# Kernel optimization log

Hardware: AMD Instinct MI355X
Metric: run time of the kernel (lower is better)

Reference implementation:

```python
import jax, jax.numpy as jnp
import numpy as np

D_MODEL = 1024
NUM_HEADS = 16
HEAD_DIM = D_MODEL // NUM_HEADS


def setup_inputs() -> dict:
    key = jax.random.key(0)
    ks = jax.random.split(key, 6)
    B, S = 2, 2048
    s = 1.0 / np.sqrt(D_MODEL)
    return {
        "x": jax.random.normal(ks[0], (B, S, D_MODEL), dtype=jnp.float32),
        "Wq": jax.random.normal(ks[1], (D_MODEL, D_MODEL), dtype=jnp.float32) * s,
        "Wk": jax.random.normal(ks[2], (D_MODEL, D_MODEL), dtype=jnp.float32) * s,
        "Wv": jax.random.normal(ks[3], (D_MODEL, D_MODEL), dtype=jnp.float32) * s,
        "Wo": jax.random.normal(ks[4], (D_MODEL, D_MODEL), dtype=jnp.float32) * s,
        "bo": jax.random.normal(ks[5], (D_MODEL,), dtype=jnp.float32) * 0.01,
    }


def reference(x, Wq, Wk, Wv, Wo, bo):
    b, n, _ = x.shape
    # QKV projections (no bias, qkv_bias=False); weights applied as x @ W^T like nn.Linear
    q = (x @ Wq.T).reshape(b, n, NUM_HEADS, HEAD_DIM).transpose(0, 2, 1, 3)  # [b,h,n,d]
    k = (x @ Wk.T).reshape(b, n, NUM_HEADS, HEAD_DIM).transpose(0, 2, 1, 3)
    v = (x @ Wv.T).reshape(b, n, NUM_HEADS, HEAD_DIM).transpose(0, 2, 1, 3)
    scores = jnp.einsum("bhqd,bhkd->bhqk", q, k)
    causal = jnp.tril(jnp.ones((n, n), dtype=bool))  # keep where True
    scores = jnp.where(causal, scores, -jnp.inf)
    weights = jax.nn.softmax(scores / np.sqrt(HEAD_DIM), axis=-1)
    # dropout p=0.0 -> identity (eval semantics)
    ctx = jnp.einsum("bhqk,bhkd->bhqd", weights, v)
    ctx = ctx.transpose(0, 2, 1, 3).reshape(b, n, D_MODEL)
    return ctx @ Wo.T + bo
```

## Files before the change

kernel.cpp:

```cpp
#include <hip/hip_runtime.h>

#define D_MODEL 1024
#define NUM_HEADS 16
#define HEAD_DIM 64
#define BATCH 2
#define SEQ 2048
#define MTOT (BATCH * SEQ)

typedef __attribute__((ext_vector_type(8))) short bf16x8;
typedef __attribute__((ext_vector_type(4))) short s16x4;
typedef __attribute__((ext_vector_type(4))) float f32x4;
typedef unsigned short u16;
typedef unsigned long long u64;

__device__ __forceinline__ u16 f2bf(float f) {
    unsigned u = __float_as_uint(f);
    return (u16)((u + 0x7FFFu + ((u >> 16) & 1u)) >> 16);
}
__device__ __forceinline__ float bf2f(u16 v) {
    return __uint_as_float((unsigned)v << 16);
}

__device__ __forceinline__ unsigned cvt_pk_bf16(float lo, float hi) {
    unsigned r;
    asm volatile("v_cvt_pk_bf16_f32 %0, %1, %2" : "=v"(r) : "v"(lo), "v"(hi));
    return r;
}

#if __has_builtin(__builtin_amdgcn_exp2f)
#define EXP2(x) __builtin_amdgcn_exp2f(x)
#else
#define EXP2(x) exp2f(x)
#endif

#define GLOAD16(gp, lp) __builtin_amdgcn_global_load_lds(                      \
    (const __attribute__((address_space(1))) void*)(gp),                       \
    (__attribute__((address_space(3))) void*)(lp), 16, 0, 0)

__global__ __launch_bounds__(256)
void cast_all_kernel(const float* __restrict__ x,  const float* __restrict__ Wq,
                     const float* __restrict__ Wk, const float* __restrict__ Wv,
                     const float* __restrict__ Wo, u16* __restrict__ dst)
{
    const int i = blockIdx.x * 256 + threadIdx.x;
    const float* src;
    int j;
    if (i < 524288) { src = x; j = i; }
    else if (i < 917504) {
        const int k = i - 524288;
        const int z = k >> 17;
        src = (z == 0) ? Wq : (z == 1) ? Wk : Wv;
        j = k & 0x1FFFF;
    } else { src = Wo; j = i - 917504; }
    const float4* s = reinterpret_cast<const float4*>(src) + (size_t)j * 2;
    float4 a = s[0], b = s[1];
    u16 tmp[8] = {f2bf(a.x), f2bf(a.y), f2bf(a.z), f2bf(a.w),
                  f2bf(b.x), f2bf(b.y), f2bf(b.z), f2bf(b.w)};
    *reinterpret_cast<int4*>(dst + (size_t)i * 8) = *reinterpret_cast<int4*>(tmp);
}

__global__ __launch_bounds__(256)
void gemm_qkv_kernel(const u16* __restrict__ A, const u16* __restrict__ B,
                     u16* __restrict__ Qo, u16* __restrict__ Ko, u16* __restrict__ Vt)
{
    __shared__ u16 Al[128 * 64];
    __shared__ u16 Bl[128 * 64];

    const int tid = threadIdx.x;
    const int l = tid & 63;
    const int w = tid >> 6;
    const int wm = w >> 1, wn = w & 1;
    const int lr = l & 15, lg = l >> 4;
    const int m0 = blockIdx.y * 128;
    const int n0 = blockIdx.x * 128;

    const int srow = tid >> 3;
    const int scol = ((tid & 7) ^ (srow & 7)) * 8;
    const int sxa = (lr & 7) * 8;

    f32x4 acc[4][4];
    #pragma unroll
    for (int i = 0; i < 4; ++i)
        #pragma unroll
        for (int j = 0; j < 4; ++j) acc[i][j] = (f32x4){0.f, 0.f, 0.f, 0.f};

    for (int k0 = 0; k0 < D_MODEL; k0 += 64) {
        __syncthreads();
        #pragma unroll
        for (int i = 0; i < 4; ++i) {
            const u16* ga = A + (size_t)(m0 + i * 32 + srow) * D_MODEL + k0 + scol;
            const u16* gb = B + (size_t)(n0 + i * 32 + srow) * D_MODEL + k0 + scol;
            GLOAD16(ga, Al + i * 2048 + w * 512);
            GLOAD16(gb, Bl + i * 2048 + w * 512);
        }
        __syncthreads();
        #pragma unroll
        for (int kc = 0; kc < 2; ++kc) {
            bf16x8 af[4], bfr[4];
            #pragma unroll
            for (int i = 0; i < 4; ++i)
                af[i] = *reinterpret_cast<const bf16x8*>(
                    &Al[(wm * 64 + i * 16 + lr) * 64 + ((kc * 32 + lg * 8) ^ sxa)]);
            #pragma unroll
            for (int j = 0; j < 4; ++j)
                bfr[j] = *reinterpret_cast<const bf16x8*>(
                    &Bl[(wn * 64 + j * 16 + lr) * 64 + ((kc * 32 + lg * 8) ^ sxa)]);
            #pragma unroll
            for (int i = 0; i < 4; ++i)
                #pragma unroll
                for (int j = 0; j < 4; ++j)
                    acc[i][j] = __builtin_amdgcn_mfma_f32_16x16x32_bf16(
                        af[i], bfr[j], acc[i][j], 0, 0, 0);
        }
    }

    const int z = (n0 >> 10);
    if (z < 2) {
        #pragma unroll
        for (int i = 0; i < 4; ++i) {
            #pragma unroll
            for (int r = 0; r < 4; ++r) {
                const int m = m0 + wm * 64 + i * 16 + lg * 4 + r;
                const int bb = m >> 11, s = m & (SEQ - 1);
                #pragma unroll
                for (int j = 0; j < 4; ++j) {
                    const int c = n0 + wn * 64 + j * 16 + lr;
                    const int cc = c & 1023, h = cc >> 6, d = cc & 63;
                    const size_t idx = ((size_t)(bb * NUM_HEADS + h) * SEQ + s) * 64 + d;
                    if (z == 0) Qo[idx] = f2bf(acc[i][j][r] * 0.18033688f);
                    else        Ko[idx] = f2bf(acc[i][j][r]);
                }
            }
        }
    } else {
        #pragma unroll
        for (int i = 0; i < 4; ++i) {
            const int mbase = m0 + wm * 64 + i * 16 + lg * 4;
            const int bb = mbase >> 11, s = mbase & (SEQ - 1);
            #pragma unroll
            for (int j = 0; j < 4; ++j) {
                const int c = n0 + wn * 64 + j * 16 + lr;
                const int cc = c & 1023, h = cc >> 6, d = cc & 63;
                u16 t4[4];
                #pragma unroll
                for (int r = 0; r < 4; ++r) t4[r] = f2bf(acc[i][j][r]);
                *reinterpret_cast<u64*>(
                    &Vt[((size_t)(bb * NUM_HEADS + h) * 64 + d) * SEQ + s]) =
                    *reinterpret_cast<u64*>(t4);
            }
        }
    }
}

__global__ __launch_bounds__(256)
void gemm_out_kernel(const u16* __restrict__ A, const u16* __restrict__ B,
                     const float* __restrict__ bias, float* __restrict__ out)
{
    __shared__ u16 Al[128 * 64];
    __shared__ u16 Bl[128 * 64];

    const int tid = threadIdx.x;
    const int l = tid & 63;
    const int w = tid >> 6;
    const int wm = w >> 1, wn = w & 1;
    const int lr = l & 15, lg = l >> 4;
    const int m0 = blockIdx.y * 128;
    const int n0 = blockIdx.x * 128;

    const int srow = tid >> 3;
    const int scol = ((tid & 7) ^ (srow & 7)) * 8;
    const int sxa = (lr & 7) * 8;

    f32x4 acc[4][4];
    #pragma unroll
    for (int i = 0; i < 4; ++i)
        #pragma unroll
        for (int j = 0; j < 4; ++j) acc[i][j] = (f32x4){0.f, 0.f, 0.f, 0.f};

    for (int k0 = 0; k0 < D_MODEL; k0 += 64) {
        __syncthreads();
        #pragma unroll
        for (int i = 0; i < 4; ++i) {
            const u16* ga = A + (size_t)(m0 + i * 32 + srow) * D_MODEL + k0 + scol;
            const u16* gb = B + (size_t)(n0 + i * 32 + srow) * D_MODEL + k0 + scol;
            GLOAD16(ga, Al + i * 2048 + w * 512);
            GLOAD16(gb, Bl + i * 2048 + w * 512);
        }
        __syncthreads();
        #pragma unroll
        for (int kc = 0; kc < 2; ++kc) {
            bf16x8 af[4], bfr[4];
            #pragma unroll
            for (int i = 0; i < 4; ++i)
                af[i] = *reinterpret_cast<const bf16x8*>(
                    &Al[(wm * 64 + i * 16 + lr) * 64 + ((kc * 32 + lg * 8) ^ sxa)]);
            #pragma unroll
            for (int j = 0; j < 4; ++j)
                bfr[j] = *reinterpret_cast<const bf16x8*>(
                    &Bl[(wn * 64 + j * 16 + lr) * 64 + ((kc * 32 + lg * 8) ^ sxa)]);
            #pragma unroll
            for (int i = 0; i < 4; ++i)
                #pragma unroll
                for (int j = 0; j < 4; ++j)
                    acc[i][j] = __builtin_amdgcn_mfma_f32_16x16x32_bf16(
                        af[i], bfr[j], acc[i][j], 0, 0, 0);
        }
    }

    #pragma unroll
    for (int i = 0; i < 4; ++i) {
        #pragma unroll
        for (int r = 0; r < 4; ++r) {
            const int m = m0 + wm * 64 + i * 16 + lg * 4 + r;
            #pragma unroll
            for (int j = 0; j < 4; ++j) {
                const int c = n0 + wn * 64 + j * 16 + lr;
                out[(size_t)m * D_MODEL + c] = acc[i][j][r] + bias[c];
            }
        }
    }
}

__device__ __forceinline__ void map_pair128(int p, int& qt2, int& ch) {
    if (p < 16)      { qt2 = 15 - (p >> 2); ch = p & 3; }
    else if (p < 28) { int t = p - 16; qt2 = 11 - t / 3; ch = t % 3; }
    else if (p < 36) { int t = p - 28; qt2 = 7 - (t >> 1); ch = t & 1; }
    else             { qt2 = 39 - p; ch = 0; }
}

__global__ __launch_bounds__(256)
void attn_kernel(const u16* __restrict__ Q, const u16* __restrict__ K,
                 const u16* __restrict__ Vt, u16* __restrict__ ctx,
                 u16* __restrict__ Opart, float* __restrict__ Lpart)
{
    __shared__ char LdsB[2][16384];

    const int tid = threadIdx.x;
    const int l = tid & 63;
    const int w = tid >> 6;
    const int lr = l & 15;
    const int lg = l >> 4;

    const int xcd  = blockIdx.x & 7;
    const int slot = blockIdx.x >> 3;
    const int bh   = xcd * 4 + slot / 40;
    int qt2, ch;
    map_pair128(slot % 40, qt2, ch);

    const int ntiles = 2 * qt2 + 2;
    const int nch  = (ntiles + 7) >> 3;
    const int base = ntiles / nch, rem = ntiles % nch;
    const int start = ch * base + (ch < rem ? ch : rem);
    const int cnt   = base + (ch < rem ? 1 : 0);

    const size_t hbase = (size_t)bh * SEQ * 64;
    const int b = bh >> 4, h = bh & (NUM_HEADS - 1);
    const u16* __restrict__ Kh = K + hbase;
    const u16* __restrict__ Vh = Vt + hbase;
    const int q0 = qt2 * 128;

    const int r0 = tid >> 3;
    const int c0 = ((tid & 7) ^ (r0 & 7)) * 8;
    const int r1 = (256 + tid) >> 3;
    const int c1 = ((tid & 7) ^ (r1 & 7)) * 8;
    const int d0b = tid * 16;
    const int d1b = 4096 + tid * 16;
    const int rswz = (lr & 7) << 4;

    bf16x8 qf[2][2];
    #pragma unroll
    for (int fq = 0; fq < 2; ++fq) {
        const u16* qp = Q + hbase + (size_t)(q0 + fq * 64 + w * 16 + lr) * 64 + lg * 8;
        qf[fq][0] = *reinterpret_cast<const bf16x8*>(qp);
        qf[fq][1] = *reinterpret_cast<const bf16x8*>(qp + 32);
    }
    asm volatile("s_waitcnt vmcnt(0)" ::: "memory");

    f32x4 acc[2][4];
    #pragma unroll
    for (int fq = 0; fq < 2; ++fq)
        #pragma unroll
        for (int nb = 0; nb < 4; ++nb) acc[fq][nb] = (f32x4){0.f, 0.f, 0.f, 0.f};
    float lsumv[2] = {0.f, 0.f};

    {
        char* kb = LdsB[0];
        char* vb = LdsB[0] + 8192;
        const int kb64 = start * 64;
        GLOAD16(Kh + (size_t)(kb64 + r0) * 64 + c0, kb + d0b);
        GLOAD16(Kh + (size_t)(kb64 + r1) * 64 + c1, kb + d1b);
        GLOAD16(Vh + (size_t)r0 * SEQ + kb64 + c0, vb + d0b);
        GLOAD16(Vh + (size_t)r1 * SEQ + kb64 + c1, vb + d1b);
    }

    for (int it = 0; it < cnt; ++it) {
        const int tile = start + it;
        const int buf = it & 1;
        if (it < cnt - 1) {
            const int kb64 = (tile + 1) * 64;
            char* kbl = LdsB[buf ^ 1];
            char* vbl = kbl + 8192;
            GLOAD16(Kh + (size_t)(kb64 + r0) * 64 + c0, kbl + d0b);
            GLOAD16(Kh + (size_t)(kb64 + r1) * 64 + c1, kbl + d1b);
            GLOAD16(Vh + (size_t)r0 * SEQ + kb64 + c0, vbl + d0b);
            GLOAD16(Vh + (size_t)r1 * SEQ + kb64 + c1, vbl + d1b);
            asm volatile("s_waitcnt vmcnt(4)" ::: "memory");
        } else {
            asm volatile("s_waitcnt vmcnt(0)" ::: "memory");
        }
        __builtin_amdgcn_s_barrier();

        const char* kbuf = LdsB[buf];
        const char* vbuf = kbuf + 8192;

        bf16x8 kf[4][2];
        #pragma unroll
        for (int m = 0; m < 4; ++m) {
            const char* krow = kbuf + (16 * m + lr) * 128;
            kf[m][0] = *reinterpret_cast<const bf16x8*>(krow + ((lg * 16) ^ rswz));
            kf[m][1] = *reinterpret_cast<const bf16x8*>(krow + ((64 + lg * 16) ^ rswz));
        }

        const bool diag = (tile >= 2 * qt2);
        const int koff0 = (tile - 2 * qt2) * 64;

        unsigned dw[2][4][2];
        __builtin_amdgcn_s_setprio(1);
        #pragma unroll
        for (int fq = 0; fq < 2; ++fq) {
            f32x4 s[4];
            #pragma unroll
            for (int m = 0; m < 4; ++m) {
                s[m] = (f32x4){0.f, 0.f, 0.f, 0.f};
                s[m] = __builtin_amdgcn_mfma_f32_16x16x32_bf16(kf[m][0], qf[fq][0], s[m], 0, 0, 0);
                s[m] = __builtin_amdgcn_mfma_f32_16x16x32_bf16(kf[m][1], qf[fq][1], s[m], 0, 0, 0);
            }
            if (diag) {
                const int qloc = fq * 64 + w * 16 + lr;
                #pragma unroll
                for (int m = 0; m < 4; ++m)
                    #pragma unroll
                    for (int r = 0; r < 4; ++r)
                        if (koff0 + 16 * m + 4 * lg + r > qloc) s[m][r] = -1.0e38f;
            }
            float p[4][4];
            #pragma unroll
            for (int m = 0; m < 4; ++m) {
                #pragma unroll
                for (int r = 0; r < 4; ++r) p[m][r] = EXP2(s[m][r]);
                lsumv[fq] += (p[m][0] + p[m][1]) + (p[m][2] + p[m][3]);
                dw[fq][m][0] = cvt_pk_bf16(p[m][0], p[m][1]);
                dw[fq][m][1] = cvt_pk_bf16(p[m][2], p[m][3]);
            }
        }

        #pragma unroll
        for (int c = 0; c < 2; ++c) {
            union Pu { unsigned u[4]; bf16x8 v; } pb[2];
            #pragma unroll
            for (int fq = 0; fq < 2; ++fq) {
                pb[fq].u[0] = dw[fq][2 * c][0];     pb[fq].u[1] = dw[fq][2 * c][1];
                pb[fq].u[2] = dw[fq][2 * c + 1][0]; pb[fq].u[3] = dw[fq][2 * c + 1][1];
            }
            #pragma unroll
            for (int nb = 0; nb < 4; ++nb) {
                const char* vrow = vbuf + (16 * nb + lr) * 128;
                union Vu { s16x4 hv[2]; bf16x8 v; } vf;
                vf.hv[0] = *reinterpret_cast<const s16x4*>(
                    vrow + ((c * 64 + lg * 8) ^ rswz));
                vf.hv[1] = *reinterpret_cast<const s16x4*>(
                    vrow + ((c * 64 + 32 + lg * 8) ^ rswz));
                acc[0][nb] = __builtin_amdgcn_mfma_f32_16x16x32_bf16(
                    vf.v, pb[0].v, acc[0][nb], 0, 0, 0);
                acc[1][nb] = __builtin_amdgcn_mfma_f32_16x16x32_bf16(
                    vf.v, pb[1].v, acc[1][nb], 0, 0, 0);
            }
        }
        __builtin_amdgcn_s_setprio(0);

        __builtin_amdgcn_s_barrier();
    }

    #pragma unroll
    for (int fq = 0; fq < 2; ++fq) {
        lsumv[fq] += __shfl_xor(lsumv[fq], 16);
        lsumv[fq] += __shfl_xor(lsumv[fq], 32);
    }

    if (nch == 1) {
        #pragma unroll
        for (int fq = 0; fq < 2; ++fq) {
            const float inv = 1.0f / lsumv[fq];
            const int qrow = q0 + fq * 64 + w * 16 + lr;
            u16* op = ctx + ((size_t)(b * SEQ) + qrow) * D_MODEL + h * 64 + 4 * lg;
            #pragma unroll
            for (int nb = 0; nb < 4; ++nb) {
                u16 t4[4];
                #pragma unroll
                for (int r = 0; r < 4; ++r) t4[r] = f2bf(acc[fq][nb][r] * inv);
                *reinterpret_cast<u64*>(op + 16 * nb) = *reinterpret_cast<u64*>(t4);
            }
        }
    } else {
        const int slot4 = ((bh * 12 + (qt2 - 4)) << 2) + ch;
        #pragma unroll
        for (int fq = 0; fq < 2; ++fq) {
            const int rloc = fq * 64 + w * 16 + lr;
            u16* op = Opart + (size_t)slot4 * 8192 + rloc * 64 + 4 * lg;
            #pragma unroll
            for (int nb = 0; nb < 4; ++nb) {
                u16 t4[4];
                #pragma unroll
                for (int r = 0; r < 4; ++r) t4[r] = f2bf(acc[fq][nb][r]);
                *reinterpret_cast<u64*>(op + 16 * nb) = *reinterpret_cast<u64*>(t4);
            }
            if (lg == 0) Lpart[slot4 * 128 + rloc] = lsumv[fq];
        }
    }
}

__global__ __launch_bounds__(128)
void attn_reduce_kernel(const u16* __restrict__ Opart,
                        const float* __restrict__ Lpart,
                        u16* __restrict__ ctx)
{
    const int blk = blockIdx.x;
    const int bh = blk / 12, idx = blk % 12;
    const int qt2 = idx + 4;
    const int nch = (2 * qt2 + 2 + 7) >> 3;
    const int t = threadIdx.x;
    const int b = bh >> 4, h = bh & (NUM_HEADS - 1);
    const int slot0 = (bh * 12 + idx) << 2;

    float acc[64] = {};
    float lt = 0.f;
    for (int ch = 0; ch < nch; ++ch) {
        const u16* op = Opart + (size_t)(slot0 + ch) * 8192 + t * 64;
        lt += Lpart[(slot0 + ch) * 128 + t];
        #pragma unroll
        for (int cchunk = 0; cchunk < 8; ++cchunk) {
            u16 v[8];
            *reinterpret_cast<int4*>(v) =
                *reinterpret_cast<const int4*>(op + cchunk * 8);
            #pragma unroll
            for (int j = 0; j < 8; ++j) acc[cchunk * 8 + j] += bf2f(v[j]);
        }
    }
    const float inv = 1.0f / lt;
    u16* orow = ctx + ((size_t)(b * SEQ) + qt2 * 128 + t) * D_MODEL + h * 64;
    #pragma unroll
    for (int cchunk = 0; cchunk < 8; ++cchunk) {
        u16 v[8];
        #pragma unroll
        for (int j = 0; j < 8; ++j) v[j] = f2bf(acc[cchunk * 8 + j] * inv);
        *reinterpret_cast<int4*>(orow + cchunk * 8) = *reinterpret_cast<int4*>(v);
    }
}


extern "C" void kernel_launch(void* const* d_in, const int* in_sizes, int n_in,
                              void* d_out, int out_size, void* d_ws, size_t ws_size,
                              hipStream_t stream)
{
    const float* x  = (const float*)d_in[0];
    const float* Wq = (const float*)d_in[1];
    const float* Wk = (const float*)d_in[2];
    const float* Wv = (const float*)d_in[3];
    const float* Wo = (const float*)d_in[4];
    const float* bo = (const float*)d_in[5];
    float* out = (float*)d_out;

    u16* xb   = (u16*)d_ws;
    u16* wqkv = xb   + (size_t)MTOT * D_MODEL;
    u16* wob  = wqkv + (size_t)3 * D_MODEL * D_MODEL;
    u16* Qw   = wob  + (size_t)D_MODEL * D_MODEL;
    u16* Kw   = Qw   + (size_t)MTOT * D_MODEL;
    u16* Vtw  = Kw   + (size_t)MTOT * D_MODEL;
    u16* ctxb = Vtw  + (size_t)MTOT * D_MODEL;
    u16* Opart = ctxb + (size_t)MTOT * D_MODEL;
    float* Lpart = (float*)(Opart + (size_t)1536 * 8192);

    cast_all_kernel<<<4096, 256, 0, stream>>>(x, Wq, Wk, Wv, Wo, xb);

    dim3 gq(3 * D_MODEL / 128, MTOT / 128);
    gemm_qkv_kernel<<<gq, 256, 0, stream>>>(xb, wqkv, Qw, Kw, Vtw);

    attn_kernel<<<dim3(1280), 256, 0, stream>>>(Qw, Kw, Vtw, ctxb, Opart, Lpart);
    attn_reduce_kernel<<<dim3(384), 128, 0, stream>>>(Opart, Lpart, ctxb);

    dim3 go(D_MODEL / 128, MTOT / 128);
    gemm_out_kernel<<<go, 256, 0, stream>>>(ctxb, wob, bo, out);
}
```

Measured before the change: 124.3 us.

## Triple-buffer QKV GEMM with 128x256 tiles, 512 threads and swizzled block order

Rewrites the QKV projection GEMM to use a 3-stage shared-memory ring with asynchronous global-to-LDS loads issued two k-steps ahead, using vmcnt waits and a single barrier per step. Tiles grow to 128x256 with 8 waves and a K step of 32, and a 1D grid with a block-index swizzle is used for L2 locality. MFMA sections are wrapped in s_setprio to favour compute issue. The goal is to hide global load latency that the previous load-sync-compute loop exposed. It costs more LDS and fewer blocks, and the epilogue indexing must still match the larger N tile.

```diff
diff --git a/kernel.cpp b/kernel.cpp
--- a/kernel.cpp
+++ b/kernel.cpp
@@ -59,24 +59,31 @@
     *reinterpret_cast<int4*>(dst + (size_t)i * 8) = *reinterpret_cast<int4*>(tmp);
 }
 
-__global__ __launch_bounds__(256)
+__global__ __launch_bounds__(512, 4)
 void gemm_qkv_kernel(const u16* __restrict__ A, const u16* __restrict__ B,
                      u16* __restrict__ Qo, u16* __restrict__ Ko, u16* __restrict__ Vt)
 {
-    __shared__ u16 Al[128 * 64];
-    __shared__ u16 Bl[128 * 64];
+    __shared__ u16 Al[3][128 * 32];
+    __shared__ u16 Bl[3][256 * 32];
 
     const int tid = threadIdx.x;
     const int l = tid & 63;
     const int w = tid >> 6;
-    const int wm = w >> 1, wn = w & 1;
+    const int wm = w >> 2, wn = w & 3;
     const int lr = l & 15, lg = l >> 4;
-    const int m0 = blockIdx.y * 128;
-    const int n0 = blockIdx.x * 128;
-
-    const int srow = tid >> 3;
-    const int scol = ((tid & 7) ^ (srow & 7)) * 8;
-    const int sxa = (lr & 7) * 8;
+
+    const int bid = blockIdx.x;
+    const int swz = (bid & 7) * 48 + (bid >> 3);
+    const int mb = swz / 12, nb = swz % 12;
+    const int m0 = mb * 128, n0 = nb * 256;
+
+    const int arow = tid >> 2;
+    const int acol = ((tid & 3) ^ ((arow >> 1) & 3)) * 8;
+    const int br1  = (512 + tid) >> 2;
+    const int bcol1 = ((tid & 3) ^ ((br1 >> 1) & 3)) * 8;
+    const int dst0 = tid * 8;
+    const int dst1 = 4096 + tid * 8;
+    const int rsw = (lr >> 1) & 3;
 
     f32x4 acc[4][4];
     #pragma unroll
@@ -84,34 +91,50 @@
         #pragma unroll
         for (int j = 0; j < 4; ++j) acc[i][j] = (f32x4){0.f, 0.f, 0.f, 0.f};
 
-    for (int k0 = 0; k0 < D_MODEL; k0 += 64) {
-        __syncthreads();
-        #pragma unroll
-        for (int i = 0; i < 4; ++i) {
-            const u16* ga = A + (size_t)(m0 + i * 32 + srow) * D_MODEL + k0 + scol;
-            const u16* gb = B + (size_t)(n0 + i * 32 + srow) * D_MODEL + k0 + scol;
-            GLOAD16(ga, Al + i * 2048 + w * 512);
-            GLOAD16(gb, Bl + i * 2048 + w * 512);
-        }
-        __syncthreads();
-        #pragma unroll
-        for (int kc = 0; kc < 2; ++kc) {
-            bf16x8 af[4], bfr[4];
-            #pragma unroll
-            for (int i = 0; i < 4; ++i)
-                af[i] = *reinterpret_cast<const bf16x8*>(
-                    &Al[(wm * 64 + i * 16 + lr) * 64 + ((kc * 32 + lg * 8) ^ sxa)]);
+    #pragma unroll
+    for (int t = 0; t < 2; ++t) {
+        const int k0 = t * 32;
+        GLOAD16(A + (size_t)(m0 + arow) * D_MODEL + k0 + acol,  &Al[t][dst0]);
+        GLOAD16(B + (size_t)(n0 + arow) * D_MODEL + k0 + acol,  &Bl[t][dst0]);
+        GLOAD16(B + (size_t)(n0 + br1)  * D_MODEL + k0 + bcol1, &Bl[t][dst1]);
+    }
+
+    int cb = 0;
+    for (int t = 0; t < 32; ++t) {
+        if (t < 31) asm volatile("s_waitcnt vmcnt(3)" ::: "memory");
+        else        asm volatile("s_waitcnt vmcnt(0)" ::: "memory");
+        __builtin_amdgcn_s_barrier();
+
+        if (t + 2 < 32) {
+            const int sb = (cb >= 1) ? cb - 1 : cb + 2;
+            const int k0 = (t + 2) * 32;
+            GLOAD16(A + (size_t)(m0 + arow) * D_MODEL + k0 + acol,  &Al[sb][dst0]);
+            GLOAD16(B + (size_t)(n0 + arow) * D_MODEL + k0 + acol,  &Bl[sb][dst0]);
+            GLOAD16(B + (size_t)(n0 + br1)  * D_MODEL + k0 + bcol1, &Bl[sb][dst1]);
+        }
+
+        const u16* __restrict__ Ab = Al[cb];
+        const u16* __restrict__ Bb = Bl[cb];
+        bf16x8 af[4], bfr[4];
+        #pragma unroll
+        for (int i = 0; i < 4; ++i)
+            af[i] = *reinterpret_cast<const bf16x8*>(
+                &Ab[(wm * 64 + i * 16 + lr) * 32 + ((lg ^ rsw) * 8)]);
+        #pragma unroll
+        for (int j = 0; j < 4; ++j)
+            bfr[j] = *reinterpret_cast<const bf16x8*>(
+                &Bb[(wn * 64 + j * 16 + lr) * 32 + ((lg ^ rsw) * 8)]);
+
+        __builtin_amdgcn_s_setprio(1);
+        #pragma unroll
+        for (int i = 0; i < 4; ++i)
             #pragma unroll
             for (int j = 0; j < 4; ++j)
-                bfr[j] = *reinterpret_cast<const bf16x8*>(
-                    &Bl[(wn * 64 + j * 16 + lr) * 64 + ((kc * 32 + lg * 8) ^ sxa)]);
-            #pragma unroll
-            for (int i = 0; i < 4; ++i)
-                #pragma unroll
-                for (int j = 0; j < 4; ++j)
-                    acc[i][j] = __builtin_amdgcn_mfma_f32_16x16x32_bf16(
-                        af[i], bfr[j], acc[i][j], 0, 0, 0);
-        }
+                acc[i][j] = __builtin_amdgcn_mfma_f32_16x16x32_bf16(
+                    af[i], bfr[j], acc[i][j], 0, 0, 0);
+        __builtin_amdgcn_s_setprio(0);
+
+        cb = (cb == 2) ? 0 : cb + 1;
     }
 
     const int z = (n0 >> 10);
@@ -482,8 +505,7 @@
 
     cast_all_kernel<<<4096, 256, 0, stream>>>(x, Wq, Wk, Wv, Wo, xb);
 
-    dim3 gq(3 * D_MODEL / 128, MTOT / 128);
-    gemm_qkv_kernel<<<gq, 256, 0, stream>>>(xb, wqkv, Qw, Kw, Vtw);
+    gemm_qkv_kernel<<<dim3(384), 512, 0, stream>>>(xb, wqkv, Qw, Kw, Vtw);
 
     attn_kernel<<<dim3(1280), 256, 0, stream>>>(Qw, Kw, Vtw, ctxb, Opart, Lpart);
     attn_reduce_kernel<<<dim3(384), 128, 0, stream>>>(Opart, Lpart, ctxb);
```

After: 118.6 us. 4.6% less time.
